# Performance work log

Hardware: AMD Instinct MI355X
Metric: run time of the kernel (lower is better)

## Reference

```python
import jax, jax.numpy as jnp
import numpy as np

# Fixed by JastrowNet source: ElectronicSchNet(n_interactions=2, kernel_dim=8, embedding_dim=16, version=1)
BATCH = 512
N_UP, N_DOWN = 16, 16
N_ELEC = N_UP + N_DOWN
N_ATOMS = 8
DIST_FEAT = 32
KERNEL = 8
EMBED = 16
N_LAYERS = 2
W_HIDDEN = 16  # log-spaced hidden dim of the w filter MLP: round(sqrt(32*8))
N_CHAN = 3     # same-spin, anti-spin, nuclear filter channels


def ssp(x):
    # shifted softplus used by SchNet
    return jax.nn.softplus(x) - jnp.log(2.0).astype(x.dtype)


def setup_inputs() -> dict:
    key = jax.random.key(0)
    ks = jax.random.split(key, 16)
    s = lambda fan_in: 1.0 / np.sqrt(fan_in)
    inp = {
        # Gaussian-expanded distance features are non-negative
        'edges_elec': jax.random.uniform(ks[0], (BATCH, N_ELEC, N_ELEC, DIST_FEAT), jnp.float32),
        'edges_nuc': jax.random.uniform(ks[1], (BATCH, N_ELEC, N_ATOMS, DIST_FEAT), jnp.float32),
        # electron spin embedding table (up=0, down=1) and nuclear embeddings Y
        'X_emb': jax.random.normal(ks[2], (2, EMBED), jnp.float32),
        'Y': jax.random.normal(ks[3], (N_ATOMS, KERNEL), jnp.float32),
        # per-layer, per-channel w filter MLP (dist_feat -> hidden -> kernel)
        'wW1': jax.random.normal(ks[4], (N_LAYERS, N_CHAN, DIST_FEAT, W_HIDDEN), jnp.float32) * s(DIST_FEAT),
        'wb1': jnp.zeros((N_LAYERS, N_CHAN, W_HIDDEN), jnp.float32),
        'wW2': jax.random.normal(ks[5], (N_LAYERS, N_CHAN, W_HIDDEN, KERNEL), jnp.float32) * s(W_HIDDEN),
        'wb2': jnp.zeros((N_LAYERS, N_CHAN, KERNEL), jnp.float32),
        # per-layer h subnet (embed -> kernel) and g subnet (kernel -> embed)
        'hW': jax.random.normal(ks[6], (N_LAYERS, EMBED, KERNEL), jnp.float32) * s(EMBED),
        'hb': jnp.zeros((N_LAYERS, KERNEL), jnp.float32),
        'gW': jax.random.normal(ks[7], (N_LAYERS, KERNEL, EMBED), jnp.float32) * s(KERNEL),
        'gb': jnp.zeros((N_LAYERS, EMBED), jnp.float32),
        # readout: Linear(16, 1, bias=False)
        'orb_W': jax.random.normal(ks[8], (EMBED,), jnp.float32) * s(EMBED),
    }
    return inp


def reference(edges_elec, edges_nuc, X_emb, Y, wW1, wb1, wW2, wb2, hW, hb, gW, gb, orb_W):
    B = edges_elec.shape[0]
    spins = jnp.concatenate([jnp.zeros(N_UP, jnp.int32), jnp.ones(N_DOWN, jnp.int32)])
    not_self = ~jnp.eye(N_ELEC, dtype=bool)
    same = ((spins[:, None] == spins[None, :]) & not_self)  # [n,n]
    anti = (spins[:, None] != spins[None, :])

    # initial electron embeddings by spin, broadcast over batch
    x = jnp.broadcast_to(X_emb[spins], (B, N_ELEC, EMBED))

    for l in range(N_LAYERS):
        def w_sub(e, c):
            h1 = ssp(e @ wW1[l, c] + wb1[l, c])
            return ssp(h1 @ wW2[l, c] + wb2[l, c])  # [..., KERNEL]

        w_same = w_sub(edges_elec, 0) * same[None, :, :, None]  # [B,n,n,k]
        w_anti = w_sub(edges_elec, 1) * anti[None, :, :, None]
        w_n = w_sub(edges_nuc, 2)                                # [B,n,m,k]

        hx = ssp(x @ hW[l] + hb[l])                              # [B,n,k]
        # continuous-filter message passing: gather neighbor features, multiply by filter, scatter-sum
        z = jnp.einsum('bijk,bjk->bik', w_same + w_anti, hx)
        z = z + jnp.einsum('bimk,mk->bik', w_n, Y)
        # version 1: single g applied to combined message, residual update
        x = x + z @ gW[l] + gb[l]

    # orbital readout Linear(16,1,bias=False).squeeze(-1).sum(-1)
    return (x @ orb_W).sum(axis=-1)  # [B]
```

## Files before the change

kernel.cpp:

```cpp
#include <hip/hip_runtime.h>
#include <hip/hip_bf16.h>
#include <cstddef>
#include <cstdint>


#define NB   512
#define NE   32
#define NA   8
#define NF   32
#define NH   16
#define NK   8
#define NEMB 16

typedef __attribute__((ext_vector_type(8))) short short8;
typedef __attribute__((ext_vector_type(4))) short short4b;
typedef __attribute__((ext_vector_type(4))) float f32x4;

#define LN2 0.69314718055994530942f

__device__ __forceinline__ float ssp(float v){
    return __logf(1.f + __expf(v)) - LN2;
}

__device__ __forceinline__ short f2bf(float x){
    unsigned b = __float_as_uint(x);
    b += 0x7fffu + ((b >> 16) & 1u);
    return (short)(b >> 16);
}
__device__ __forceinline__ unsigned packbf2(float lo, float hi){
    return (unsigned)(unsigned short)f2bf(lo) | ((unsigned)(unsigned short)f2bf(hi) << 16);
}
__device__ __forceinline__ short8 cvt_row(float4 a, float4 b){
    short8 s;
    s[0]=f2bf(a.x); s[1]=f2bf(a.y); s[2]=f2bf(a.z); s[3]=f2bf(a.w);
    s[4]=f2bf(b.x); s[5]=f2bf(b.y); s[6]=f2bf(b.z); s[7]=f2bf(b.w);
    return s;
}

__device__ __forceinline__ f32x4 mfma16x16(short4b a, short4b b, f32x4 c){
#if __has_builtin(__builtin_amdgcn_mfma_f32_16x16x16bf16_1k)
    return __builtin_amdgcn_mfma_f32_16x16x16bf16_1k(a, b, c, 0, 0, 0);
#else
    f32x4 d;
    asm("s_nop 1\n\tv_mfma_f32_16x16x16_bf16 %0, %1, %2, %3\n\ts_nop 7"
        : "=v"(d) : "v"(a), "v"(b), "v"(c));
    return d;
#endif
}

extern "C" __global__ void __launch_bounds__(1024, 4)
jastrow_kernel(const float* __restrict__ edges_elec,
               const float* __restrict__ edges_nuc,
               const float* __restrict__ X_emb,
               const float* __restrict__ Yk,
               const float* __restrict__ wW1, const float* __restrict__ wb1,
               const float* __restrict__ wW2, const float* __restrict__ wb2,
               const float* __restrict__ hW,  const float* __restrict__ hb,
               const float* __restrict__ gW,  const float* __restrict__ gb,
               const float* __restrict__ orbW,
               float* __restrict__ out)
{
    __shared__ __align__(16) __hip_bfloat16 s_w2[NE*NE*NK];
    __shared__ __align__(16) float s_z1p[2*NE*NK];
    __shared__ __align__(16) float s_zn1[NE*NK];
    __shared__ __align__(16) float s_zn2[NE*NK];
    __shared__ float s_hx1[2*NK];
    __shared__ float s_x[NE*NEMB];
    __shared__ float s_z[NE*NK];
    __shared__ float s_hx[NE*NK];
    __shared__ float s_red[16];
    __shared__ __align__(16) short s_w1T[3][2][NH][NF];
    __shared__ __align__(16) short s_w2T[3][2][16][NH];
    __shared__ __align__(16) float s_b1[3][2][NH];
    __shared__ __align__(16) float s_b2[3][2][16];

    const int b = blockIdx.x, t = threadIdx.x;
    const int wid = t >> 6, lane = t & 63;
    const int r16 = lane & 15, g4 = lane >> 4;

    const int ccE = wid & 1;
    const int wq  = (wid >> 1) * 4;
    auto esrc = [&](int u) -> const float* {
        const int tau = wq + u;
        const int qi = tau >> 4, g = tau & 15;
        const int qj = ccE ? (1 - qi) : qi;
        return edges_elec + (((size_t)b*NE + qi*16 + g)*NE + qj*16 + r16)*NF + g4*8;
    };
    float4 ra = ((const float4*)esrc(0))[0];
    float4 rb = ((const float4*)esrc(0))[1];
    const int nm = lane & 7;
    const int ni = 2*wid + (r16 >> 3);
    const float* nsrc = edges_nuc + (((size_t)b*NE + ni)*NA + nm)*NF + g4*8;
    const float4 nra = ((const float4*)nsrc)[0];
    const float4 nrb = ((const float4*)nsrc)[1];

    for (int idx = t; idx < 3*2*NH*NF; idx += 1024){
        const int f = idx & 31, h = (idx >> 5) & 15;
        const int l = (idx >> 9) & 1, cc = idx >> 10;
        s_w1T[cc][l][h][f] = f2bf(wW1[((size_t)(l*3 + cc)*NF + f)*NH + h]);
    }
    for (int idx = t; idx < 3*2*16*NH; idx += 1024){
        const int h = idx & 15, k = (idx >> 4) & 15;
        const int l = (idx >> 8) & 1, cc = idx >> 9;
        s_w2T[cc][l][k][h] = (k < NK)
            ? f2bf(wW2[((size_t)(l*3 + cc)*NH + h)*NK + k]) : (short)0;
    }
    if (t < 3*2*NH){
        const int m = t & 15, l = (t >> 4) & 1, cc = t >> 5;
        s_b1[cc][l][m] = wb1[(l*3 + cc)*NH + m];
        s_b2[cc][l][m] = (m < NK) ? wb2[(l*3 + cc)*NK + m] : 0.f;
    }
    if (t >= 1008){
        const int tt = t - 1008;
        const int s = tt >> 3, k = tt & 7;
        float acc = hb[k];
#pragma unroll
        for (int e = 0; e < NEMB; e++)
            acc = fmaf(X_emb[s*NEMB + e], hW[e*NK + k], acc);
        s_hx1[tt] = ssp(acc);
    }
    __syncthreads();

    short8 a1[2]; short4b a2[2]; f32x4 c1[2], c2[2];
#pragma unroll
    for (int l = 0; l < 2; l++){
        a1[l] = *(const short8*)&s_w1T[ccE][l][r16][g4*8];
        a2[l] = *(const short4b*)&s_w2T[ccE][l][r16][g4*4];
        c1[l] = *(const f32x4*)&s_b1[ccE][l][g4*4];
        c2[l] = *(const f32x4*)&s_b2[ccE][l][g4*4];
    }

#pragma unroll
    for (int u = 0; u < 4; u++){
        float4 nxa = ra, nxb = rb;
        if (u < 3){
            const float* src = esrc(u + 1);
            nxa = ((const float4*)src)[0];
            nxb = ((const float4*)src)[1];
        }
        const int tau = wq + u;
        const int qi = tau >> 4, g = tau & 15;
        const int qj = ccE ? (1 - qi) : qi;
        const int i  = qi*16 + g;
        const short8 bfr = cvt_row(ra, rb);
#pragma unroll
        for (int l = 0; l < 2; l++){
            f32x4 d1 = __builtin_amdgcn_mfma_f32_16x16x32_bf16(a1[l], bfr, c1[l], 0, 0, 0);
            short4b bb;
            bb[0] = f2bf(ssp(d1[0]));
            bb[1] = f2bf(ssp(d1[1]));
            bb[2] = f2bf(ssp(d1[2]));
            bb[3] = f2bf(ssp(d1[3]));
            f32x4 d2 = mfma16x16(a2[l], bb, c2[l]);
            float wk[4];
#pragma unroll
            for (int r = 0; r < 4; r++) wk[r] = ssp(d2[r]);
            if (ccE == 0 && r16 == g){
#pragma unroll
                for (int r = 0; r < 4; r++) wk[r] = 0.f;
            }
            if (l == 0){
#pragma unroll
                for (int off = 1; off < 16; off <<= 1)
#pragma unroll
                    for (int r = 0; r < 4; r++) wk[r] += __shfl_xor(wk[r], off, 64);
                if (r16 == 0 && g4 < 2){
                    float4 st;
                    st.x = wk[0]*s_hx1[qj*NK + g4*4 + 0];
                    st.y = wk[1]*s_hx1[qj*NK + g4*4 + 1];
                    st.z = wk[2]*s_hx1[qj*NK + g4*4 + 2];
                    st.w = wk[3]*s_hx1[qj*NK + g4*4 + 3];
                    *(float4*)&s_z1p[(qj*NE + i)*NK + g4*4] = st;
                }
            } else if (g4 < 2){
                const int j = qj*16 + r16;
                uint2 uu;
                uu.x = packbf2(wk[0], wk[1]);
                uu.y = packbf2(wk[2], wk[3]);
                *(uint2*)&s_w2[(i*NE + j)*NK + g4*4] = uu;
            }
        }
        ra = nxa; rb = nxb;
    }

    {
#pragma unroll
        for (int l = 0; l < 2; l++){
            a1[l] = *(const short8*)&s_w1T[2][l][r16][g4*8];
            a2[l] = *(const short4b*)&s_w2T[2][l][r16][g4*4];
            c1[l] = *(const f32x4*)&s_b1[2][l][g4*4];
            c2[l] = *(const f32x4*)&s_b2[2][l][g4*4];
        }
        float Yv[4];
#pragma unroll
        for (int r = 0; r < 4; r++)
            Yv[r] = Yk[nm*NK + ((g4*4 + r) & 7)];
        const short8 bfr = cvt_row(nra, nrb);
#pragma unroll
        for (int l = 0; l < 2; l++){
            f32x4 d1 = __builtin_amdgcn_mfma_f32_16x16x32_bf16(a1[l], bfr, c1[l], 0, 0, 0);
            short4b bb;
            bb[0] = f2bf(ssp(d1[0]));
            bb[1] = f2bf(ssp(d1[1]));
            bb[2] = f2bf(ssp(d1[2]));
            bb[3] = f2bf(ssp(d1[3]));
            f32x4 d2 = mfma16x16(a2[l], bb, c2[l]);
            float wk[4];
#pragma unroll
            for (int r = 0; r < 4; r++) wk[r] = ssp(d2[r]) * Yv[r];
#pragma unroll
            for (int off = 1; off < 8; off <<= 1)
#pragma unroll
                for (int r = 0; r < 4; r++) wk[r] += __shfl_xor(wk[r], off, 64);
            if ((r16 & 7) == 0 && g4 < 2){
                float* dst = l ? s_zn2 : s_zn1;
                float4 st; st.x = wk[0]; st.y = wk[1]; st.z = wk[2]; st.w = wk[3];
                *(float4*)&dst[ni*NK + g4*4] = st;
            }
        }
    }
    __syncthreads();

    if (t < NE*NEMB){
        const int i = t >> 4, e = t & 15;
        float acc = gb[e];
#pragma unroll
        for (int k = 0; k < NK; k++){
            const float zk = s_z1p[i*NK + k] + s_z1p[NE*NK + i*NK + k]
                           + s_zn1[i*NK + k];
            acc = fmaf(zk, gW[k*NEMB + e], acc);
        }
        s_x[t] = X_emb[(i >> 4)*NEMB + e] + acc;
    }
    __syncthreads();
    if (t < NE*NK){
        const int i = t >> 3, k = t & 7;
        float acc = hb[NK + k];
#pragma unroll
        for (int e = 0; e < NEMB; e++)
            acc = fmaf(s_x[i*NEMB + e], hW[NEMB*NK + e*NK + k], acc);
        s_hx[t] = ssp(acc);
    }
    __syncthreads();
    if (t < NE*NEMB){
        const int i = t >> 4, j16 = t & 15;
        float zacc[NK];
#pragma unroll
        for (int k = 0; k < NK; k++) zacc[k] = 0.f;
#pragma unroll
        for (int qj = 0; qj < 2; qj++){
            const int j = qj*16 + j16;
            union { uint4 u; __hip_bfloat16 h[8]; } raw;
            raw.u = *(const uint4*)&s_w2[((size_t)i*NE + j)*NK];
            float pk[NK];
#pragma unroll
            for (int k = 0; k < NK; k++)
                pk[k] = __bfloat162float(raw.h[k]) * s_hx[j*NK + k];
#pragma unroll
            for (int off = 8; off > 0; off >>= 1)
#pragma unroll
                for (int k = 0; k < NK; k++) pk[k] += __shfl_down(pk[k], off, 16);
#pragma unroll
            for (int k = 0; k < NK; k++) zacc[k] += pk[k];
        }
        if (j16 == 0){
#pragma unroll
            for (int k = 0; k < NK; k++)
                s_z[i*NK + k] = zacc[k] + s_zn2[i*NK + k];
        }
    }
    __syncthreads();
    if (t < NE*NEMB){
        const int i = t >> 4, e = t & 15;
        float acc = gb[NEMB + e];
#pragma unroll
        for (int k = 0; k < NK; k++)
            acc = fmaf(s_z[i*NK + k], gW[NK*NEMB + k*NEMB + e], acc);
        s_x[t] += acc;
    }
    __syncthreads();
    float part = (t < NE*NEMB) ? s_x[t] * orbW[t & 15] : 0.f;
#pragma unroll
    for (int off = 32; off > 0; off >>= 1) part += __shfl_down(part, off, 64);
    if (lane == 0) s_red[wid] = part;
    __syncthreads();
    if (t == 0){
        float r = 0.f;
#pragma unroll
        for (int w = 0; w < 16; w++) r += s_red[w];
        out[b] = r;
    }
}

extern "C" void kernel_launch(void* const* d_in, const int* in_sizes, int n_in,
                              void* d_out, int out_size, void* d_ws, size_t ws_size,
                              hipStream_t stream)
{
    const float* edges_elec = (const float*)d_in[0];
    const float* edges_nuc  = (const float*)d_in[1];
    const float* X_emb      = (const float*)d_in[2];
    const float* Yk         = (const float*)d_in[3];
    const float* wW1        = (const float*)d_in[4];
    const float* wb1        = (const float*)d_in[5];
    const float* wW2        = (const float*)d_in[6];
    const float* wb2        = (const float*)d_in[7];
    const float* hW         = (const float*)d_in[8];
    const float* hb         = (const float*)d_in[9];
    const float* gW         = (const float*)d_in[10];
    const float* gb         = (const float*)d_in[11];
    const float* orbW       = (const float*)d_in[12];

    jastrow_kernel<<<NB, 1024, 0, stream>>>(
        edges_elec, edges_nuc, X_emb, Yk, wW1, wb1, wW2, wb2, hW, hb,
        gW, gb, orbW, (float*)d_out);
}
```

Before: 152.0 us.

## Store all filter outputs to padded LDS and reduce per (i,k) thread

Instead of reducing layer-1 and nuclear filter outputs with cross-lane shuffles inside the MFMA loop, every filter value (both layers, electron and nuclear) is now written as bf16 into padded shared-memory tiles. A separate pass then has one thread per (electron, kernel) sum over neighbors and atoms. The aim is to remove the shuffle-reduction chains from the hot filter loop and to avoid bank conflicts through padded strides. The cost is more LDS traffic, an extra barrier and serial per-thread loops over 32 neighbors, with only 256 threads active during those reductions.

```diff
diff --git a/kernel.cpp b/kernel.cpp
--- a/kernel.cpp
+++ b/kernel.cpp
@@ -12,6 +12,9 @@
 #define NK   8
 #define NEMB 16
 
+#define W_STRIDE  264
+#define WN_STRIDE 72
+
 typedef __attribute__((ext_vector_type(8))) short short8;
 typedef __attribute__((ext_vector_type(4))) short short4b;
 typedef __attribute__((ext_vector_type(4))) float f32x4;
@@ -29,6 +32,9 @@
 }
 __device__ __forceinline__ unsigned packbf2(float lo, float hi){
     return (unsigned)(unsigned short)f2bf(lo) | ((unsigned)(unsigned short)f2bf(hi) << 16);
+}
+__device__ __forceinline__ float bf2f(short s){
+    return __uint_as_float(((unsigned)(unsigned short)s) << 16);
 }
 __device__ __forceinline__ short8 cvt_row(float4 a, float4 b){
     short8 s;
@@ -60,11 +66,11 @@
                const float* __restrict__ orbW,
                float* __restrict__ out)
 {
-    __shared__ __align__(16) __hip_bfloat16 s_w2[NE*NE*NK];
-    __shared__ __align__(16) float s_z1p[2*NE*NK];
-    __shared__ __align__(16) float s_zn1[NE*NK];
-    __shared__ __align__(16) float s_zn2[NE*NK];
+    __shared__ __align__(16) short s_w1[NE*W_STRIDE];
+    __shared__ __align__(16) short s_w2[NE*W_STRIDE];
+    __shared__ __align__(16) short s_wn[2][NE*WN_STRIDE];
     __shared__ float s_hx1[2*NK];
+    __shared__ float s_Y[NA*NK];
     __shared__ float s_x[NE*NEMB];
     __shared__ float s_z[NE*NK];
     __shared__ float s_hx[NE*NK];
@@ -110,6 +116,8 @@
         s_b1[cc][l][m] = wb1[(l*3 + cc)*NH + m];
         s_b2[cc][l][m] = (m < NK) ? wb2[(l*3 + cc)*NK + m] : 0.f;
     }
+    if (t >= 896 && t < 896 + NA*NK)
+        s_Y[t - 896] = Yk[t - 896];
     if (t >= 1008){
         const int tt = t - 1008;
         const int s = tt >> 3, k = tt & 7;
@@ -142,6 +150,7 @@
         const int qi = tau >> 4, g = tau & 15;
         const int qj = ccE ? (1 - qi) : qi;
         const int i  = qi*16 + g;
+        const int j  = qj*16 + r16;
         const short8 bfr = cvt_row(ra, rb);
 #pragma unroll
         for (int l = 0; l < 2; l++){
@@ -159,25 +168,12 @@
 #pragma unroll
                 for (int r = 0; r < 4; r++) wk[r] = 0.f;
             }
-            if (l == 0){
-#pragma unroll
-                for (int off = 1; off < 16; off <<= 1)
-#pragma unroll
-                    for (int r = 0; r < 4; r++) wk[r] += __shfl_xor(wk[r], off, 64);
-                if (r16 == 0 && g4 < 2){
-                    float4 st;
-                    st.x = wk[0]*s_hx1[qj*NK + g4*4 + 0];
-                    st.y = wk[1]*s_hx1[qj*NK + g4*4 + 1];
-                    st.z = wk[2]*s_hx1[qj*NK + g4*4 + 2];
-                    st.w = wk[3]*s_hx1[qj*NK + g4*4 + 3];
-                    *(float4*)&s_z1p[(qj*NE + i)*NK + g4*4] = st;
-                }
-            } else if (g4 < 2){
-                const int j = qj*16 + r16;
+            if (g4 < 2){
+                short* dst = l ? s_w2 : s_w1;
                 uint2 uu;
                 uu.x = packbf2(wk[0], wk[1]);
                 uu.y = packbf2(wk[2], wk[3]);
-                *(uint2*)&s_w2[(i*NE + j)*NK + g4*4] = uu;
+                *(uint2*)&dst[i*W_STRIDE + j*NK + g4*4] = uu;
             }
         }
         ra = nxa; rb = nxb;
@@ -191,10 +187,6 @@
             c1[l] = *(const f32x4*)&s_b1[2][l][g4*4];
             c2[l] = *(const f32x4*)&s_b2[2][l][g4*4];
         }
-        float Yv[4];
-#pragma unroll
-        for (int r = 0; r < 4; r++)
-            Yv[r] = Yk[nm*NK + ((g4*4 + r) & 7)];
         const short8 bfr = cvt_row(nra, nrb);
 #pragma unroll
         for (int l = 0; l < 2; l++){
@@ -205,31 +197,37 @@
             bb[2] = f2bf(ssp(d1[2]));
             bb[3] = f2bf(ssp(d1[3]));
             f32x4 d2 = mfma16x16(a2[l], bb, c2[l]);
-            float wk[4];
-#pragma unroll
-            for (int r = 0; r < 4; r++) wk[r] = ssp(d2[r]) * Yv[r];
-#pragma unroll
-            for (int off = 1; off < 8; off <<= 1)
-#pragma unroll
-                for (int r = 0; r < 4; r++) wk[r] += __shfl_xor(wk[r], off, 64);
-            if ((r16 & 7) == 0 && g4 < 2){
-                float* dst = l ? s_zn2 : s_zn1;
-                float4 st; st.x = wk[0]; st.y = wk[1]; st.z = wk[2]; st.w = wk[3];
-                *(float4*)&dst[ni*NK + g4*4] = st;
+            if (g4 < 2){
+                uint2 uu;
+                uu.x = packbf2(ssp(d2[0]), ssp(d2[1]));
+                uu.y = packbf2(ssp(d2[2]), ssp(d2[3]));
+                *(uint2*)&s_wn[l][ni*WN_STRIDE + nm*NK + g4*4] = uu;
             }
         }
     }
     __syncthreads();
 
+    if (t < NE*NK){
+        const int i = t >> 3, k = t & 7;
+        float p0 = 0.f, p1 = 0.f;
+#pragma unroll
+        for (int j = 0; j < 16; j++){
+            p0 += bf2f(s_w1[i*W_STRIDE + j*NK + k]);
+            p1 += bf2f(s_w1[i*W_STRIDE + (16 + j)*NK + k]);
+        }
+        float z1 = p0*s_hx1[k] + p1*s_hx1[NK + k];
+#pragma unroll
+        for (int m = 0; m < NA; m++)
+            z1 = fmaf(bf2f(s_wn[0][i*WN_STRIDE + m*NK + k]), s_Y[m*NK + k], z1);
+        s_z[t] = z1;
+    }
+    __syncthreads();
     if (t < NE*NEMB){
         const int i = t >> 4, e = t & 15;
         float acc = gb[e];
 #pragma unroll
-        for (int k = 0; k < NK; k++){
-            const float zk = s_z1p[i*NK + k] + s_z1p[NE*NK + i*NK + k]
-                           + s_zn1[i*NK + k];
-            acc = fmaf(zk, gW[k*NEMB + e], acc);
-        }
+        for (int k = 0; k < NK; k++)
+            acc = fmaf(s_z[i*NK + k], gW[k*NEMB + e], acc);
         s_x[t] = X_emb[(i >> 4)*NEMB + e] + acc;
     }
     __syncthreads();
@@ -242,32 +240,16 @@
         s_hx[t] = ssp(acc);
     }
     __syncthreads();
-    if (t < NE*NEMB){
-        const int i = t >> 4, j16 = t & 15;
-        float zacc[NK];
-#pragma unroll
-        for (int k = 0; k < NK; k++) zacc[k] = 0.f;
-#pragma unroll
-        for (int qj = 0; qj < 2; qj++){
-            const int j = qj*16 + j16;
-            union { uint4 u; __hip_bfloat16 h[8]; } raw;
-            raw.u = *(const uint4*)&s_w2[((size_t)i*NE + j)*NK];
-            float pk[NK];
-#pragma unroll
-            for (int k = 0; k < NK; k++)
-                pk[k] = __bfloat162float(raw.h[k]) * s_hx[j*NK + k];
-#pragma unroll
-            for (int off = 8; off > 0; off >>= 1)
-#pragma unroll
-                for (int k = 0; k < NK; k++) pk[k] += __shfl_down(pk[k], off, 16);
-#pragma unroll
-            for (int k = 0; k < NK; k++) zacc[k] += pk[k];
-        }
-        if (j16 == 0){
-#pragma unroll
-            for (int k = 0; k < NK; k++)
-                s_z[i*NK + k] = zacc[k] + s_zn2[i*NK + k];
-        }
+    if (t < NE*NK){
+        const int i = t >> 3, k = t & 7;
+        float z2 = 0.f;
+#pragma unroll
+        for (int j = 0; j < NE; j++)
+            z2 = fmaf(bf2f(s_w2[i*W_STRIDE + j*NK + k]), s_hx[j*NK + k], z2);
+#pragma unroll
+        for (int m = 0; m < NA; m++)
+            z2 = fmaf(bf2f(s_wn[1][i*WN_STRIDE + m*NK + k]), s_Y[m*NK + k], z2);
+        s_z[t] = z2;
     }
     __syncthreads();
     if (t < NE*NEMB){
```

After: 147.5 us. -2.9%, faster.
